# Kernel optimization log

Measured on AMD Instinct MI355X. Metric: run time of the kernel, lower is better.

The kernel has to match this reference:

```python
import jax, jax.numpy as jnp
import numpy as np

B, T, C, HEAD = 4, 4096, 1024, 64
SCALE = 1.0 / (C ** 0.5)  # module divides by embedding_size**0.5, not head_size**0.5


def setup_inputs() -> dict:
    key = jax.random.key(0)
    kx, kq, kk, kv = jax.random.split(key, 4)
    x = jax.random.normal(kx, (B, T, C), dtype=jnp.float32)
    # nn.Linear(C, head_size, bias=False) weights, stored as (C, head_size) for x @ W
    Wq = jax.random.normal(kq, (C, HEAD), dtype=jnp.float32) * (1.0 / np.sqrt(C))
    Wk = jax.random.normal(kk, (C, HEAD), dtype=jnp.float32) * (1.0 / np.sqrt(C))
    Wv = jax.random.normal(kv, (C, HEAD), dtype=jnp.float32) * (1.0 / np.sqrt(C))
    return {"x": x, "Wq": Wq, "Wk": Wk, "Wv": Wv}


def reference(x, Wq, Wk, Wv):
    q = jnp.einsum('btc,ch->bth', x, Wq)  # [B,T,HEAD]
    k = jnp.einsum('btc,ch->bth', x, Wk)
    v = jnp.einsum('btc,ch->bth', x, Wv)
    aff = jnp.einsum('bqh,bkh->bqk', q, k) * SCALE  # [B,T,T]
    causal = jnp.tril(jnp.ones((T, T), dtype=bool))
    aff = jnp.where(causal, aff, -jnp.inf)
    p = jax.nn.softmax(aff, axis=-1)  # dropout p=0.0 -> identity
    return jnp.einsum('bqk,bkh->bqh', p, v)  # [B,T,HEAD]
```

## Files before the change

### kernel.cpp

```cpp
#include <hip/hip_runtime.h>

#define T_SEQ 4096
#define NBATCH 4
#define CDIM 1024
#define NHEAD 64
#define SCALE (1.0f / 32.0f)
#define LOG2E 1.4426950408889634f
#define BT (NBATCH * T_SEQ)
#define NW 8
#define WREG 8960

typedef __bf16 bf16x8 __attribute__((ext_vector_type(8)));
typedef float f32x4 __attribute__((ext_vector_type(4)));
typedef float f32x16 __attribute__((ext_vector_type(16)));

__device__ __forceinline__ unsigned short f2bf(float f) {
  union { float f; unsigned u; } x;
  x.f = f;
  unsigned r = x.u + 0x7FFFu + ((x.u >> 16) & 1u);
  return (unsigned short)(r >> 16);
}

__device__ __forceinline__ unsigned cvt_pk(float lo, float hi) {
  unsigned d;
  asm("v_cvt_pk_bf16_f32 %0, %1, %2" : "=v"(d) : "v"(lo), "v"(hi));
  return d;
}

__device__ __forceinline__ void swap32(unsigned& a, unsigned& b) {
  asm("v_permlane32_swap_b32 %0, %1" : "+v"(a), "+v"(b));
}

__device__ __forceinline__ f32x4 mfma16(bf16x8 a, bf16x8 b, f32x4 c) {
  return __builtin_amdgcn_mfma_f32_16x16x32_bf16(a, b, c, 0, 0, 0);
}

__device__ __forceinline__ f32x16 mfma32(bf16x8 a, bf16x8 b, f32x16 c) {
  return __builtin_amdgcn_mfma_f32_32x32x16_bf16(a, b, c, 0, 0, 0);
}

__global__ void prep_w(const float* __restrict__ Wq, const float* __restrict__ Wk,
                       const float* __restrict__ Wv, unsigned short* __restrict__ Wt) {
  int c = blockIdx.x;
  const float* W = (c < 64) ? Wq : (c < 128) ? Wk : Wv;
  int cc = c & 63;
  float sc = (c < 64) ? (SCALE * LOG2E) : 1.0f;
  for (int k = threadIdx.x; k < CDIM; k += blockDim.x)
    Wt[c * CDIM + k] = f2bf(W[k * NHEAD + cc] * sc);
}

__global__ __launch_bounds__(256) void proj_qkv(
    const float* __restrict__ x, const unsigned short* __restrict__ Wt,
    unsigned short* __restrict__ qws, unsigned short* __restrict__ kws,
    unsigned short* __restrict__ vtws) {
  __shared__ unsigned short xlds[2][16][136];
  const int tid = threadIdx.x;
  const int lane = tid & 63;
  const int w = tid >> 6;
  const int g = lane >> 4;
  const int c15 = lane & 15;
  const int rb = blockIdx.x * 16;

  f32x4 acc[3];
  for (int j = 0; j < 3; j++) acc[j] = (f32x4){0.f, 0.f, 0.f, 0.f};

  const int sr = tid >> 4;
  const int scc = (tid & 15) * 8;
  const float* xrow = x + (size_t)(rb + sr) * CDIM + scc;

  {
    float4 c0 = *(const float4*)(xrow);
    float4 c1 = *(const float4*)(xrow + 4);
    unsigned short pk[8];
    pk[0] = f2bf(c0.x); pk[1] = f2bf(c0.y); pk[2] = f2bf(c0.z); pk[3] = f2bf(c0.w);
    pk[4] = f2bf(c1.x); pk[5] = f2bf(c1.y); pk[6] = f2bf(c1.z); pk[7] = f2bf(c1.w);
    *(bf16x8*)&xlds[0][sr][scc] = *(bf16x8*)pk;
  }
  __syncthreads();

  int pb = 0;
  for (int k0 = 0; k0 < CDIM; k0 += 128) {
    const bool more = (k0 + 128 < CDIM);
    float4 n0, n1;
    if (more) {
      n0 = *(const float4*)(xrow + k0 + 128);
      n1 = *(const float4*)(xrow + k0 + 132);
    }

    bf16x8 wfrag[4][3];
    for (int kk = 0; kk < 4; kk++)
      for (int bn = 0; bn < 3; bn++) {
        int col = w * 48 + bn * 16 + c15;
        wfrag[kk][bn] =
            *(const bf16x8*)&Wt[(size_t)col * CDIM + k0 + kk * 32 + g * 8];
      }

    for (int kk = 0; kk < 4; kk++) {
      bf16x8 a = *(bf16x8*)&xlds[pb][c15][kk * 32 + g * 8];
      for (int bn = 0; bn < 3; bn++)
        acc[bn] = mfma16(a, wfrag[kk][bn], acc[bn]);
    }

    if (more) {
      unsigned short pk[8];
      pk[0] = f2bf(n0.x); pk[1] = f2bf(n0.y); pk[2] = f2bf(n0.z); pk[3] = f2bf(n0.w);
      pk[4] = f2bf(n1.x); pk[5] = f2bf(n1.y); pk[6] = f2bf(n1.z); pk[7] = f2bf(n1.w);
      *(bf16x8*)&xlds[pb ^ 1][sr][scc] = *(bf16x8*)pk;
    }
    __syncthreads();
    pb ^= 1;
  }

  for (int bn = 0; bn < 3; bn++) {
    int col = w * 48 + bn * 16 + c15;
    for (int r = 0; r < 4; r++) {
      unsigned short v = f2bf(acc[bn][r]);
      int t = rb + 4 * g + r;
      if (col < 64)
        qws[(size_t)t * 64 + col] = v;
      else if (col < 128)
        kws[(size_t)t * 64 + (col - 64)] = v;
      else
        vtws[(size_t)(col - 128) * BT + t] = v;
    }
  }
}

__global__ __launch_bounds__(512, 2) void attn_fwd(
    const unsigned short* __restrict__ qws, const unsigned short* __restrict__ kws,
    const unsigned short* __restrict__ vtws, float* __restrict__ out) {
  __shared__ __align__(16) char smem[NW * WREG];
  const int tid = threadIdx.x;
  const int lane = tid & 63;
  const int w = tid >> 6;
  const int q31 = lane & 31;
  const int hi = lane >> 5;
  const int b = blockIdx.x >> 6;
  const int pi = blockIdx.x & 63;
  const size_t rowbase = (size_t)b * T_SEQ;
  char* wbase = smem + w * WREG;

  for (int half = 0; half < 2; ++half) {
    const int qt = half ? (127 - pi) : pi;
    const int qb = qt * 32;
    const int nsteps = qt + 1;

    bf16x8 qf[4];
    for (int h2 = 0; h2 < 4; h2++)
      qf[h2] = *(const bf16x8*)&qws[(rowbase + qb + q31) * 64 + h2 * 16 + hi * 8];

    f32x16 o[2];
    o[0] = (f32x16)0.f;
    o[1] = (f32x16)0.f;
    float mrow = -1e30f;
    float lrun = 0.f;

    for (int st = w; st < nsteps; st += NW) {
      const int kt = st * 32;
      bf16x8 ka[4];
      for (int h2 = 0; h2 < 4; h2++)
        ka[h2] =
            *(const bf16x8*)&kws[(rowbase + kt + q31) * 64 + h2 * 16 + hi * 8];
      bf16x8 va[2][2];
      for (int nt = 0; nt < 2; nt++)
        for (int ki = 0; ki < 2; ki++)
          va[nt][ki] = *(const bf16x8*)&vtws[(size_t)(nt * 32 + q31) * BT +
                                             rowbase + kt + ki * 16 + hi * 8];

      f32x16 s = (f32x16)0.f;
      for (int h2 = 0; h2 < 4; h2++) s = mfma32(ka[h2], qf[h2], s);

      float sv[16];
      for (int r = 0; r < 16; r++) sv[r] = s[r];

      if (st == nsteps - 1) {
        for (int r = 0; r < 16; r++) {
          int key = kt + (r & 3) + 8 * (r >> 2) + 4 * hi;
          if (key > qb + q31) sv[r] = -1e30f;
        }
      }

      float t01 = fmaxf(sv[0], sv[1]), t23 = fmaxf(sv[2], sv[3]);
      float t45 = fmaxf(sv[4], sv[5]), t67 = fmaxf(sv[6], sv[7]);
      float t89 = fmaxf(sv[8], sv[9]), tab = fmaxf(sv[10], sv[11]);
      float tcd = fmaxf(sv[12], sv[13]), tef = fmaxf(sv[14], sv[15]);
      float t = fmaxf(fmaxf(fmaxf(t01, t23), fmaxf(t45, t67)),
                      fmaxf(fmaxf(t89, tab), fmaxf(tcd, tef)));
      t = fmaxf(t, __shfl_xor(t, 32));

      float mn = fmaxf(mrow, t);
      float a = exp2f(mrow - mn);
      mrow = mn;
      o[0] *= a;
      o[1] *= a;
      lrun *= a;

      float p[16];
      for (int r = 0; r < 16; r++) p[r] = exp2f(sv[r] - mrow);

      float ssum = 0.f;
      for (int r = 0; r < 16; r++) ssum += p[r];
      lrun += ssum + __shfl_xor(ssum, 32);

      unsigned X[8];
      for (int jj = 0; jj < 8; jj++) X[jj] = cvt_pk(p[2 * jj], p[2 * jj + 1]);
      swap32(X[0], X[2]);
      swap32(X[1], X[3]);
      swap32(X[4], X[6]);
      swap32(X[5], X[7]);

      union { unsigned u[4]; bf16x8 v; } bf0, bf1;
      bf0.u[0] = X[0]; bf0.u[1] = X[1]; bf0.u[2] = X[2]; bf0.u[3] = X[3];
      bf1.u[0] = X[4]; bf1.u[1] = X[5]; bf1.u[2] = X[6]; bf1.u[3] = X[7];

      for (int nt = 0; nt < 2; nt++) {
        o[nt] = mfma32(va[nt][0], bf0.v, o[nt]);
        o[nt] = mfma32(va[nt][1], bf1.v, o[nt]);
      }
    }

    float* ow = (float*)wbase;
    float* mw = (float*)(wbase + 8704);
    float* lw = (float*)(wbase + 8832);
    for (int nt = 0; nt < 2; nt++)
      for (int r = 0; r < 16; r++) {
        int d = nt * 32 + (r & 3) + 8 * (r >> 2) + 4 * hi;
        ow[q31 * 68 + d] = o[nt][r];
      }
    if (hi == 0) {
      mw[q31] = mrow;
      lw[q31] = lrun;
    }
    __syncthreads();

    for (int i = 0; i < 4; i++) {
      int e = tid + i * 512;
      int row = e >> 6;
      int d = e & 63;
      float M = -1e30f;
      for (int ww = 0; ww < NW; ww++)
        M = fmaxf(M, ((const float*)(smem + ww * WREG + 8704))[row]);
      float L = 0.f, O = 0.f;
      for (int ww = 0; ww < NW; ww++) {
        float mv = ((const float*)(smem + ww * WREG + 8704))[row];
        float f = exp2f(mv - M);
        L += f * ((const float*)(smem + ww * WREG + 8832))[row];
        O += f * ((const float*)(smem + ww * WREG))[row * 68 + d];
      }
      out[(rowbase + qb + row) * 64 + d] = O / L;
    }
    __syncthreads();
  }
}

extern "C" void kernel_launch(void* const* d_in, const int* in_sizes, int n_in,
                              void* d_out, int out_size, void* d_ws, size_t ws_size,
                              hipStream_t stream) {
  const float* x = (const float*)d_in[0];
  const float* Wq = (const float*)d_in[1];
  const float* Wk = (const float*)d_in[2];
  const float* Wv = (const float*)d_in[3];
  float* out = (float*)d_out;

  char* ws = (char*)d_ws;
  unsigned short* Wt = (unsigned short*)(ws);
  unsigned short* qws = (unsigned short*)(ws + 393216);
  unsigned short* kws = (unsigned short*)(ws + 393216 + 2097152);
  unsigned short* vtws = (unsigned short*)(ws + 393216 + 2 * 2097152);

  prep_w<<<dim3(192), dim3(256), 0, stream>>>(Wq, Wk, Wv, Wt);
  proj_qkv<<<dim3(1024), dim3(256), 0, stream>>>(x, Wt, qws, kws, vtws);
  attn_fwd<<<dim3(256), dim3(512), 0, stream>>>(qws, kws, vtws, out);
}
```

Measured before the change: 95.33 us.

## Rewrite QKV projection as single-wave blocks with register double-buffering, no LDS

The projection kernel now runs one 64-lane wave per 16-row block. That wave computes all 192 output columns across 12 accumulators, loading x and W fragments directly from global memory into registers. It double-buffers these loads across k-chunks instead of staging x through shared memory with block barriers, which removes the LDS traffic and __syncthreads. The cost is many more registers per lane, and far fewer waves in flight (1024 single-wave blocks) to hide global memory latency.

```diff
diff --git a/kernel.cpp b/kernel.cpp
--- a/kernel.cpp
+++ b/kernel.cpp
@@ -49,72 +49,74 @@
     Wt[c * CDIM + k] = f2bf(W[k * NHEAD + cc] * sc);
 }
 
-__global__ __launch_bounds__(256) void proj_qkv(
+__global__ __launch_bounds__(64, 1) void proj_qkv(
     const float* __restrict__ x, const unsigned short* __restrict__ Wt,
     unsigned short* __restrict__ qws, unsigned short* __restrict__ kws,
     unsigned short* __restrict__ vtws) {
-  __shared__ unsigned short xlds[2][16][136];
-  const int tid = threadIdx.x;
-  const int lane = tid & 63;
-  const int w = tid >> 6;
+  const int lane = threadIdx.x;
+  const int c15 = lane & 15;
   const int g = lane >> 4;
-  const int c15 = lane & 15;
   const int rb = blockIdx.x * 16;
-
-  f32x4 acc[3];
-  for (int j = 0; j < 3; j++) acc[j] = (f32x4){0.f, 0.f, 0.f, 0.f};
-
-  const int sr = tid >> 4;
-  const int scc = (tid & 15) * 8;
-  const float* xrow = x + (size_t)(rb + sr) * CDIM + scc;
-
-  {
-    float4 c0 = *(const float4*)(xrow);
-    float4 c1 = *(const float4*)(xrow + 4);
-    unsigned short pk[8];
-    pk[0] = f2bf(c0.x); pk[1] = f2bf(c0.y); pk[2] = f2bf(c0.z); pk[3] = f2bf(c0.w);
-    pk[4] = f2bf(c1.x); pk[5] = f2bf(c1.y); pk[6] = f2bf(c1.z); pk[7] = f2bf(c1.w);
-    *(bf16x8*)&xlds[0][sr][scc] = *(bf16x8*)pk;
+  const float* xrow = x + (size_t)(rb + c15) * CDIM + g * 8;
+  const unsigned short* wbase = Wt + (size_t)c15 * CDIM + g * 8;
+
+  f32x4 acc[12];
+#pragma unroll
+  for (int ct = 0; ct < 12; ct++) acc[ct] = (f32x4){0.f, 0.f, 0.f, 0.f};
+
+  float4 xa[2], xb[2];
+  bf16x8 wa[12], wb[12];
+
+  xa[0] = *(const float4*)(xrow);
+  xa[1] = *(const float4*)(xrow + 4);
+#pragma unroll
+  for (int ct = 0; ct < 12; ct++)
+    wa[ct] = *(const bf16x8*)&wbase[(size_t)ct * 16 * CDIM];
+
+  for (int ch = 0; ch < 32; ch += 2) {
+    {
+      const int k1 = (ch + 1) * 32;
+      xb[0] = *(const float4*)(xrow + k1);
+      xb[1] = *(const float4*)(xrow + k1 + 4);
+#pragma unroll
+      for (int ct = 0; ct < 12; ct++)
+        wb[ct] = *(const bf16x8*)&wbase[(size_t)ct * 16 * CDIM + k1];
+    }
+    {
+      union { unsigned u[4]; bf16x8 v; } av;
+      av.u[0] = cvt_pk(xa[0].x, xa[0].y);
+      av.u[1] = cvt_pk(xa[0].z, xa[0].w);
+      av.u[2] = cvt_pk(xa[1].x, xa[1].y);
+      av.u[3] = cvt_pk(xa[1].z, xa[1].w);
+#pragma unroll
+      for (int ct = 0; ct < 12; ct++)
+        acc[ct] = mfma16(av.v, wa[ct], acc[ct]);
+    }
+    if (ch + 2 < 32) {
+      const int k2 = (ch + 2) * 32;
+      xa[0] = *(const float4*)(xrow + k2);
+      xa[1] = *(const float4*)(xrow + k2 + 4);
+#pragma unroll
+      for (int ct = 0; ct < 12; ct++)
+        wa[ct] = *(const bf16x8*)&wbase[(size_t)ct * 16 * CDIM + k2];
+    }
+    {
+      union { unsigned u[4]; bf16x8 v; } av;
+      av.u[0] = cvt_pk(xb[0].x, xb[0].y);
+      av.u[1] = cvt_pk(xb[0].z, xb[0].w);
+      av.u[2] = cvt_pk(xb[1].x, xb[1].y);
+      av.u[3] = cvt_pk(xb[1].z, xb[1].w);
+#pragma unroll
+      for (int ct = 0; ct < 12; ct++)
+        acc[ct] = mfma16(av.v, wb[ct], acc[ct]);
+    }
   }
-  __syncthreads();
-
-  int pb = 0;
-  for (int k0 = 0; k0 < CDIM; k0 += 128) {
-    const bool more = (k0 + 128 < CDIM);
-    float4 n0, n1;
-    if (more) {
-      n0 = *(const float4*)(xrow + k0 + 128);
-      n1 = *(const float4*)(xrow + k0 + 132);
-    }
-
-    bf16x8 wfrag[4][3];
-    for (int kk = 0; kk < 4; kk++)
-      for (int bn = 0; bn < 3; bn++) {
-        int col = w * 48 + bn * 16 + c15;
-        wfrag[kk][bn] =
-            *(const bf16x8*)&Wt[(size_t)col * CDIM + k0 + kk * 32 + g * 8];
-      }
-
-    for (int kk = 0; kk < 4; kk++) {
-      bf16x8 a = *(bf16x8*)&xlds[pb][c15][kk * 32 + g * 8];
-      for (int bn = 0; bn < 3; bn++)
-        acc[bn] = mfma16(a, wfrag[kk][bn], acc[bn]);
-    }
-
-    if (more) {
-      unsigned short pk[8];
-      pk[0] = f2bf(n0.x); pk[1] = f2bf(n0.y); pk[2] = f2bf(n0.z); pk[3] = f2bf(n0.w);
-      pk[4] = f2bf(n1.x); pk[5] = f2bf(n1.y); pk[6] = f2bf(n1.z); pk[7] = f2bf(n1.w);
-      *(bf16x8*)&xlds[pb ^ 1][sr][scc] = *(bf16x8*)pk;
-    }
-    __syncthreads();
-    pb ^= 1;
-  }
-
-  for (int bn = 0; bn < 3; bn++) {
-    int col = w * 48 + bn * 16 + c15;
+
+#pragma unroll
+  for (int ct = 0; ct < 12; ct++) {
+    int col = ct * 16 + c15;
     for (int r = 0; r < 4; r++) {
-      unsigned short v = f2bf(acc[bn][r]);
+      unsigned short v = f2bf(acc[ct][r]);
       int t = rb + 4 * g + r;
       if (col < 64)
         qws[(size_t)t * 64 + col] = v;
@@ -269,6 +271,6 @@
   unsigned short* vtws = (unsigned short*)(ws + 393216 + 2 * 2097152);
 
   prep_w<<<dim3(192), dim3(256), 0, stream>>>(Wq, Wk, Wv, Wt);
-  proj_qkv<<<dim3(1024), dim3(256), 0, stream>>>(x, Wt, qws, kws, vtws);
+  proj_qkv<<<dim3(1024), dim3(64), 0, stream>>>(x, Wt, qws, kws, vtws);
   attn_fwd<<<dim3(256), dim3(512), 0, stream>>>(qws, kws, vtws, out);
 }
```

After: 105.9 us. 11.0% more time.
